# Kernel optimization log

Measured on AMD Instinct MI355X. Metric: run time of the kernel, lower is better.

## Reference

```python
import jax, jax.numpy as jnp
import numpy as np

D_MODEL = 1024  # scale uses sqrt(d_model), matching the source's sqrt(C)

def setup_inputs() -> dict:
    key = jax.random.key(0)
    kx, kq, kk, kv = jax.random.split(key, 4)
    B, T, C, H = 8, 2048, D_MODEL, 64
    s = 1.0 / np.sqrt(C)
    return {
        "x": jax.random.normal(kx, (B, T, C), dtype=jnp.float32),
        "Wq": jax.random.normal(kq, (C, H), dtype=jnp.float32) * s,
        "Wk": jax.random.normal(kk, (C, H), dtype=jnp.float32) * s,
        "Wv": jax.random.normal(kv, (C, H), dtype=jnp.float32) * s,
    }

def reference(x, Wq, Wk, Wv):
    B, T, C = x.shape
    q = jnp.einsum("btc,ch->bth", x, Wq)
    k = jnp.einsum("btc,ch->bth", x, Wk)
    v = jnp.einsum("btc,ch->bth", x, Wv)
    # scores scaled by 1/sqrt(C) (C = d_model), faithful to source
    wei = jnp.einsum("bth,bsh->bts", q, k) / jnp.sqrt(jnp.float32(C))
    causal = jnp.tril(jnp.ones((T, T), dtype=bool))  # [T, T]
    wei = jnp.where(causal, wei, -jnp.inf)
    wei = jax.nn.softmax(wei, axis=-1)
    out = jnp.einsum("bts,bsh->bth", wei, v)
    return out
```

## Files before the change

### kernel.cpp

```cpp
#include <hip/hip_runtime.h>

typedef unsigned short u16;
typedef __attribute__((ext_vector_type(4))) float f32x4;
typedef __attribute__((ext_vector_type(8))) short bf16x8;
typedef __attribute__((ext_vector_type(4))) u16 u16x4;

#define MFMA(a, b, c) __builtin_amdgcn_mfma_f32_16x16x32_bf16(a, b, c, 0, 0, 0)

__device__ __forceinline__ u16 f2bf(float f) {
    unsigned u = __float_as_uint(f);
    u += 0x7fffu + ((u >> 16) & 1u);
    return (u16)(u >> 16);
}

__device__ __forceinline__ void load_lds16(const void* g, void* l) {
    __builtin_amdgcn_global_load_lds((const __attribute__((address_space(1))) void*)g,
                                     (__attribute__((address_space(3))) void*)l,
                                     16, 0, 0);
}

__global__ void wt_pack(const float* __restrict__ Wq, const float* __restrict__ Wk,
                        const float* __restrict__ Wv, u16* __restrict__ Wtt) {
    const int k = blockIdx.x;
    const int n = threadIdx.x;
    const float* W = (n < 64) ? Wq : (n < 128 ? Wk : Wv);
    const float v = W[(size_t)k * 64 + (n & 63)];
    const int kt = k >> 6, ks = k & 63, c = ks >> 3, ci = ks & 7;
    Wtt[(size_t)kt * 12288 + n * 64 + (((c ^ (n & 7)) << 3) + ci)] = f2bf(v);
}

__global__ __launch_bounds__(256, 2) void qkv_gemm(const float* __restrict__ x,
                                                   const u16* __restrict__ Wtt,
                                                   u16* __restrict__ qo,
                                                   u16* __restrict__ ko,
                                                   u16* __restrict__ vT) {
    const int tid = threadIdx.x;
    const int lane = tid & 63, wave = tid >> 6;
    const int lr = lane & 15, lg = lane >> 4;
    const int m0 = blockIdx.x * 32;

    __shared__ __align__(16) float xs[2][32 * 64];
    __shared__ __align__(16) u16 ws[2][192 * 64];

    f32x4 acc[2][3];
#pragma unroll
    for (int m = 0; m < 2; ++m)
#pragma unroll
        for (int n = 0; n < 3; ++n) acc[m][n] = (f32x4){0.f, 0.f, 0.f, 0.f};

    const int srow = tid >> 4;
    const int schk = tid & 15;

    {
#pragma unroll
        for (int j = 0; j < 2; ++j) {
            const int rr = j * 16 + srow;
            const float* src = x + (size_t)(m0 + rr) * 1024 + ((schk ^ (rr & 7)) << 2);
            load_lds16(src, &xs[0][j * 1024 + wave * 256]);
        }
#pragma unroll
        for (int j = 0; j < 6; ++j) {
            const u16* src = Wtt + (size_t)j * 2048 + tid * 8;
            load_lds16(src, &ws[0][j * 2048 + wave * 512]);
        }
    }
    __syncthreads();

    for (int kt = 0; kt < 16; ++kt) {
        const int cur = kt & 1;
        if (kt < 15) {
            const int nxt = cur ^ 1;
#pragma unroll
            for (int j = 0; j < 2; ++j) {
                const int rr = j * 16 + srow;
                const float* src =
                    x + (size_t)(m0 + rr) * 1024 + (kt + 1) * 64 + ((schk ^ (rr & 7)) << 2);
                load_lds16(src, &xs[nxt][j * 1024 + wave * 256]);
            }
#pragma unroll
            for (int j = 0; j < 6; ++j) {
                const u16* src = Wtt + (size_t)(kt + 1) * 12288 + j * 2048 + tid * 8;
                load_lds16(src, &ws[nxt][j * 2048 + wave * 512]);
            }
        }
#pragma unroll
        for (int h = 0; h < 2; ++h) {
            bf16x8 a[2];
#pragma unroll
            for (int mm = 0; mm < 2; ++mm) {
                const int rr = mm * 16 + lr;
                const int c0 = h * 8 + lg * 2;
                f32x4 f0 = *(const f32x4*)&xs[cur][rr * 64 + ((c0 ^ (rr & 7)) << 2)];
                f32x4 f1 = *(const f32x4*)&xs[cur][rr * 64 + (((c0 + 1) ^ (rr & 7)) << 2)];
                bf16x8 t;
#pragma unroll
                for (int i = 0; i < 4; ++i) {
                    t[i] = (short)f2bf(f0[i]);
                    t[i + 4] = (short)f2bf(f1[i]);
                }
                a[mm] = t;
            }
#pragma unroll
            for (int nl = 0; nl < 3; ++nl) {
                const int row = (wave * 3 + nl) * 16 + lr;
                const int cb = h * 4 + lg;
                const bf16x8 b = *(const bf16x8*)&ws[cur][row * 64 + ((cb ^ (row & 7)) << 3)];
                acc[0][nl] = MFMA(a[0], b, acc[0][nl]);
                acc[1][nl] = MFMA(a[1], b, acc[1][nl]);
            }
        }
        __syncthreads();
    }

    const float SCQ = 0.0450842200277801f;
    const int bb = m0 >> 11;
    const int tb = m0 & 2047;
#pragma unroll
    for (int mm = 0; mm < 2; ++mm)
#pragma unroll
        for (int nl = 0; nl < 3; ++nl) {
            const int col = (wave * 3 + nl) * 16 + lr;
            const int rl = mm * 16 + lg * 4;
            if (col < 64) {
#pragma unroll
                for (int r = 0; r < 4; ++r)
                    qo[(size_t)(m0 + rl + r) * 64 + col] = f2bf(acc[mm][nl][r] * SCQ);
            } else if (col < 128) {
#pragma unroll
                for (int r = 0; r < 4; ++r)
                    ko[(size_t)(m0 + rl + r) * 64 + (col - 64)] = f2bf(acc[mm][nl][r]);
            } else {
                u16x4 pk;
#pragma unroll
                for (int r = 0; r < 4; ++r) pk[r] = f2bf(acc[mm][nl][r]);
                *(u16x4*)&vT[(size_t)(bb * 64 + (col - 128)) * 2048 + tb + rl] = pk;
            }
        }
}

#define PPITCH 72
__global__ __launch_bounds__(256, 2) void attn_part(const u16* __restrict__ q,
                                                    const u16* __restrict__ k,
                                                    const u16* __restrict__ vT,
                                                    float* __restrict__ Op,
                                                    float* __restrict__ Lp) {
    const int b = blockIdx.x & 7;
    int g = blockIdx.x >> 3;
    int qt = 31, rem = g;
    while (rem >= (qt >> 3) + 1) { rem -= (qt >> 3) + 1; --qt; }
    const int c0 = rem;
    const int q0 = qt * 64;
    const int kv_lo = c0 * 512;
    const int kv_hi = min(kv_lo + 512, q0 + 64);
    const int ntiles = (kv_hi - kv_lo) >> 6;
    const int slot = (b * 32 + qt) * 4 + c0;

    __shared__ __align__(16) u16 lK[2][64 * 64];
    __shared__ __align__(16) u16 lV[2][64 * 64];
    __shared__ __align__(16) u16 lP[4][16 * PPITCH];

    const int tid = threadIdx.x;
    const int wave = tid >> 6, lane = tid & 63;
    const int lr = lane & 15, lg = lane >> 4;

    const u16* qb = q + (size_t)b * 2048 * 64;
    const u16* kb = k + (size_t)b * 2048 * 64;
    const u16* vb = vT + (size_t)b * 64 * 2048;

    const int myrow = q0 + wave * 16 + lr;
    const bf16x8 qf0 = *(const bf16x8*)(qb + (size_t)myrow * 64 + lg * 8);
    const bf16x8 qf1 = *(const bf16x8*)(qb + (size_t)myrow * 64 + 32 + lg * 8);

    f32x4 oacc[4];
#pragma unroll
    for (int n = 0; n < 4; ++n) oacc[n] = (f32x4){0.f, 0.f, 0.f, 0.f};
    float rs = 0.f;

#define STAGE(bufi, kv0_)                                                             \
    {                                                                                 \
        _Pragma("unroll") for (int j = 0; j < 2; ++j) {                               \
            const int cid = j * 256 + wave * 64 + lane;                               \
            const int row = cid >> 3, cc = cid & 7;                                   \
            load_lds16(kb + (size_t)((kv0_) + row) * 64 + ((cc ^ (row & 7)) << 3),    \
                       &lK[bufi][(j * 256 + wave * 64) * 8]);                         \
            load_lds16(vb + (size_t)row * 2048 + (kv0_) + ((cc ^ (row & 7)) << 3),    \
                       &lV[bufi][(j * 256 + wave * 64) * 8]);                         \
        }                                                                             \
    }

    STAGE(0, kv_lo);
    __syncthreads();

    for (int it = 0; it < ntiles; ++it) {
        const int cur = it & 1;
        if (it + 1 < ntiles) STAGE(cur ^ 1, kv_lo + (it + 1) * 64);

        const int kv0 = kv_lo + it * 64;
        if (kv0 <= q0 + wave * 16 + 15) {
            f32x4 s[4];
#pragma unroll
            for (int n = 0; n < 4; ++n) {
                const int row = n * 16 + lr;
                const bf16x8 kf0 = *(const bf16x8*)&lK[cur][row * 64 + ((lg ^ (row & 7)) << 3)];
                const bf16x8 kf1 =
                    *(const bf16x8*)&lK[cur][row * 64 + (((4 + lg) ^ (row & 7)) << 3)];
                f32x4 a = (f32x4){0.f, 0.f, 0.f, 0.f};
                a = MFMA(kf0, qf0, a);
                a = MFMA(kf1, qf1, a);
                s[n] = a;
            }

            const bool msk = (kv0 + 63 > q0 + wave * 16);
#pragma unroll
            for (int n = 0; n < 4; ++n) {
                u16x4 pk;
#pragma unroll
                for (int r = 0; r < 4; ++r) {
                    const int kvi = kv0 + n * 16 + lg * 4 + r;
                    const float p = (!msk || kvi <= myrow) ? exp2f(s[n][r]) : 0.f;
                    rs += p;
                    pk[r] = f2bf(p);
                }
                *(u16x4*)&lP[wave][lr * PPITCH + n * 16 + lg * 4] = pk;
            }

#pragma unroll
            for (int kc = 0; kc < 2; ++kc) {
                const bf16x8 pf = *(const bf16x8*)&lP[wave][lr * PPITCH + kc * 32 + lg * 8];
#pragma unroll
                for (int n = 0; n < 4; ++n) {
                    const int row = n * 16 + lr;
                    const bf16x8 vf =
                        *(const bf16x8*)&lV[cur][row * 64 + (((kc * 4 + lg) ^ (row & 7)) << 3)];
                    oacc[n] = MFMA(pf, vf, oacc[n]);
                }
            }
        }
        __syncthreads();
    }

    rs += __shfl_xor(rs, 16);
    rs += __shfl_xor(rs, 32);
    if (lane < 16) Lp[slot * 64 + wave * 16 + lr] = rs;

    float* op = Op + (size_t)slot * 4096;
#pragma unroll
    for (int n = 0; n < 4; ++n)
#pragma unroll
        for (int r = 0; r < 4; ++r)
            op[(wave * 16 + lg * 4 + r) * 64 + n * 16 + lr] = oacc[n][r];
}

__global__ __launch_bounds__(256) void attn_combine(const float* __restrict__ Op,
                                                    const float* __restrict__ Lp,
                                                    float* __restrict__ out) {
    const int gid = blockIdx.x * 256 + threadIdx.x;
    const int col = gid & 63;
    const int row = gid >> 6;
    const int b = row >> 11, tt = row & 2047;
    const int qt = tt >> 6, i = tt & 63;
    const int nc = (qt >> 3) + 1;
    const size_t sbase = (size_t)(b * 32 + qt) * 4;

    float O = 0.f, L = 0.f;
    for (int c = 0; c < nc; ++c) {
        O += Op[(sbase + c) * 4096 + i * 64 + col];
        L += Lp[(sbase + c) * 64 + i];
    }
    out[(size_t)row * 64 + col] = O / L;
}

extern "C" void kernel_launch(void* const* d_in, const int* in_sizes, int n_in,
                              void* d_out, int out_size, void* d_ws, size_t ws_size,
                              hipStream_t stream) {
    const float* x = (const float*)d_in[0];
    const float* Wq = (const float*)d_in[1];
    const float* Wk = (const float*)d_in[2];
    const float* Wv = (const float*)d_in[3];
    float* out = (float*)d_out;

    char* ws = (char*)d_ws;
    u16* Wtt = (u16*)ws;
    u16* qb = (u16*)(ws + (512 << 10));
    u16* kb = (u16*)(ws + (512 << 10) + (2 << 20));
    u16* vT = (u16*)(ws + (512 << 10) + (4 << 20));
    float* Op = (float*)(ws + (8 << 20));
    float* Lp = (float*)(ws + (25 << 20));

    wt_pack<<<1024, 192, 0, stream>>>(Wq, Wk, Wv, Wtt);
    qkv_gemm<<<512, 256, 0, stream>>>(x, Wtt, qb, kb, vT);
    attn_part<<<640, 256, 0, stream>>>(qb, kb, vT, Op, Lp);
    attn_combine<<<4096, 256, 0, stream>>>(Op, Lp, out);
}
```

Baseline: 57.21 us.

## Enlarge GEMM and attention KV tiles and store partial outputs as bf16

The QKV GEMM now uses 512-thread blocks covering 64 rows, so each staged weight tile is shared by twice as many rows. The attention kernel stages 128 KV rows per iteration instead of 64, which halves the number of barriers and loop trips. Partial attention outputs are written as bf16 in a tiled layout, cutting the write and read traffic of the combine pass. The trade-offs are more LDS per block, which may lower occupancy, and some precision lost in the partial sums.

```diff
diff --git a/kernel.cpp b/kernel.cpp
--- a/kernel.cpp
+++ b/kernel.cpp
@@ -11,6 +11,10 @@
     unsigned u = __float_as_uint(f);
     u += 0x7fffu + ((u >> 16) & 1u);
     return (u16)(u >> 16);
+}
+__device__ __forceinline__ float bf2f(u16 h) {
+    unsigned u = ((unsigned)h) << 16;
+    return __uint_as_float(u);
 }
 
 __device__ __forceinline__ void load_lds16(const void* g, void* l) {
@@ -29,7 +33,7 @@
     Wtt[(size_t)kt * 12288 + n * 64 + (((c ^ (n & 7)) << 3) + ci)] = f2bf(v);
 }
 
-__global__ __launch_bounds__(256, 2) void qkv_gemm(const float* __restrict__ x,
+__global__ __launch_bounds__(512, 2) void qkv_gemm(const float* __restrict__ x,
                                                    const u16* __restrict__ Wtt,
                                                    u16* __restrict__ qo,
                                                    u16* __restrict__ ko,
@@ -37,9 +41,10 @@
     const int tid = threadIdx.x;
     const int lane = tid & 63, wave = tid >> 6;
     const int lr = lane & 15, lg = lane >> 4;
-    const int m0 = blockIdx.x * 32;
-
-    __shared__ __align__(16) float xs[2][32 * 64];
+    const int wr = wave >> 2, wc = wave & 3;
+    const int m0 = blockIdx.x * 64;
+
+    __shared__ __align__(16) float xs[2][64 * 64];
     __shared__ __align__(16) u16 ws[2][192 * 64];
 
     f32x4 acc[2][3];
@@ -48,47 +53,34 @@
 #pragma unroll
         for (int n = 0; n < 3; ++n) acc[m][n] = (f32x4){0.f, 0.f, 0.f, 0.f};
 
-    const int srow = tid >> 4;
-    const int schk = tid & 15;
-
-    {
-#pragma unroll
-        for (int j = 0; j < 2; ++j) {
-            const int rr = j * 16 + srow;
-            const float* src = x + (size_t)(m0 + rr) * 1024 + ((schk ^ (rr & 7)) << 2);
-            load_lds16(src, &xs[0][j * 1024 + wave * 256]);
-        }
-#pragma unroll
-        for (int j = 0; j < 6; ++j) {
-            const u16* src = Wtt + (size_t)j * 2048 + tid * 8;
-            load_lds16(src, &ws[0][j * 2048 + wave * 512]);
-        }
-    }
+#define QSTAGE(bufi, kt_)                                                              \
+    {                                                                                  \
+        _Pragma("unroll") for (int j = 0; j < 2; ++j) {                                \
+            const int cid = j * 512 + tid;                                             \
+            const int row = cid >> 4, cc = cid & 15;                                   \
+            load_lds16(x + (size_t)(m0 + row) * 1024 + (kt_)*64 +                      \
+                           ((cc ^ (row & 7)) << 2),                                    \
+                       &xs[bufi][(j * 512 + wave * 64) * 4]);                          \
+        }                                                                              \
+        _Pragma("unroll") for (int j = 0; j < 3; ++j) {                                \
+            const int cid = j * 512 + tid;                                             \
+            load_lds16(Wtt + (size_t)(kt_)*12288 + cid * 8,                            \
+                       &ws[bufi][(j * 512 + wave * 64) * 8]);                          \
+        }                                                                              \
+    }
+
+    QSTAGE(0, 0);
     __syncthreads();
 
     for (int kt = 0; kt < 16; ++kt) {
         const int cur = kt & 1;
-        if (kt < 15) {
-            const int nxt = cur ^ 1;
-#pragma unroll
-            for (int j = 0; j < 2; ++j) {
-                const int rr = j * 16 + srow;
-                const float* src =
-                    x + (size_t)(m0 + rr) * 1024 + (kt + 1) * 64 + ((schk ^ (rr & 7)) << 2);
-                load_lds16(src, &xs[nxt][j * 1024 + wave * 256]);
-            }
-#pragma unroll
-            for (int j = 0; j < 6; ++j) {
-                const u16* src = Wtt + (size_t)(kt + 1) * 12288 + j * 2048 + tid * 8;
-                load_lds16(src, &ws[nxt][j * 2048 + wave * 512]);
-            }
-        }
+        if (kt < 15) QSTAGE(cur ^ 1, kt + 1);
 #pragma unroll
         for (int h = 0; h < 2; ++h) {
             bf16x8 a[2];
 #pragma unroll
             for (int mm = 0; mm < 2; ++mm) {
-                const int rr = mm * 16 + lr;
+                const int rr = wr * 32 + mm * 16 + lr;
                 const int c0 = h * 8 + lg * 2;
                 f32x4 f0 = *(const f32x4*)&xs[cur][rr * 64 + ((c0 ^ (rr & 7)) << 2)];
                 f32x4 f1 = *(const f32x4*)&xs[cur][rr * 64 + (((c0 + 1) ^ (rr & 7)) << 2)];
@@ -102,7 +94,7 @@
             }
 #pragma unroll
             for (int nl = 0; nl < 3; ++nl) {
-                const int row = (wave * 3 + nl) * 16 + lr;
+                const int row = wc * 48 + nl * 16 + lr;
                 const int cb = h * 4 + lg;
                 const bf16x8 b = *(const bf16x8*)&ws[cur][row * 64 + ((cb ^ (row & 7)) << 3)];
                 acc[0][nl] = MFMA(a[0], b, acc[0][nl]);
@@ -119,8 +111,8 @@
     for (int mm = 0; mm < 2; ++mm)
 #pragma unroll
         for (int nl = 0; nl < 3; ++nl) {
-            const int col = (wave * 3 + nl) * 16 + lr;
-            const int rl = mm * 16 + lg * 4;
+            const int col = wc * 48 + nl * 16 + lr;
+            const int rl = wr * 32 + mm * 16 + lg * 4;
             if (col < 64) {
 #pragma unroll
                 for (int r = 0; r < 4; ++r)
@@ -142,7 +134,7 @@
 __global__ __launch_bounds__(256, 2) void attn_part(const u16* __restrict__ q,
                                                     const u16* __restrict__ k,
                                                     const u16* __restrict__ vT,
-                                                    float* __restrict__ Op,
+                                                    u16* __restrict__ Opb,
                                                     float* __restrict__ Lp) {
     const int b = blockIdx.x & 7;
     int g = blockIdx.x >> 3;
@@ -152,11 +144,11 @@
     const int q0 = qt * 64;
     const int kv_lo = c0 * 512;
     const int kv_hi = min(kv_lo + 512, q0 + 64);
-    const int ntiles = (kv_hi - kv_lo) >> 6;
+    const int niter = (kv_hi - kv_lo + 127) >> 7;
     const int slot = (b * 32 + qt) * 4 + c0;
 
-    __shared__ __align__(16) u16 lK[2][64 * 64];
-    __shared__ __align__(16) u16 lV[2][64 * 64];
+    __shared__ __align__(16) u16 lK[2][128 * 64];
+    __shared__ __align__(16) u16 lV[2][64 * 128];
     __shared__ __align__(16) u16 lP[4][16 * PPITCH];
 
     const int tid = threadIdx.x;
@@ -176,63 +168,71 @@
     for (int n = 0; n < 4; ++n) oacc[n] = (f32x4){0.f, 0.f, 0.f, 0.f};
     float rs = 0.f;
 
-#define STAGE(bufi, kv0_)                                                             \
-    {                                                                                 \
-        _Pragma("unroll") for (int j = 0; j < 2; ++j) {                               \
-            const int cid = j * 256 + wave * 64 + lane;                               \
-            const int row = cid >> 3, cc = cid & 7;                                   \
-            load_lds16(kb + (size_t)((kv0_) + row) * 64 + ((cc ^ (row & 7)) << 3),    \
-                       &lK[bufi][(j * 256 + wave * 64) * 8]);                         \
-            load_lds16(vb + (size_t)row * 2048 + (kv0_) + ((cc ^ (row & 7)) << 3),    \
-                       &lV[bufi][(j * 256 + wave * 64) * 8]);                         \
-        }                                                                             \
-    }
-
-    STAGE(0, kv_lo);
+#define ASTAGE(bufi, kv0_)                                                             \
+    {                                                                                  \
+        _Pragma("unroll") for (int j = 0; j < 4; ++j) {                                \
+            const int cid = j * 256 + tid;                                             \
+            const int krow = cid >> 3, kcc = cid & 7;                                  \
+            load_lds16(kb + (size_t)((kv0_) + krow) * 64 + ((kcc ^ (krow & 7)) << 3),  \
+                       &lK[bufi][(j * 256 + wave * 64) * 8]);                          \
+            const int vrow = cid >> 4, vcc = cid & 15;                                 \
+            const int vsw = (vcc & 8) | ((vcc & 7) ^ (vrow & 7));                      \
+            load_lds16(vb + (size_t)vrow * 2048 + (kv0_) + (vsw << 3),                 \
+                       &lV[bufi][(j * 256 + wave * 64) * 8]);                          \
+        }                                                                              \
+    }
+
+    ASTAGE(0, kv_lo);
     __syncthreads();
 
-    for (int it = 0; it < ntiles; ++it) {
+    for (int it = 0; it < niter; ++it) {
         const int cur = it & 1;
-        if (it + 1 < ntiles) STAGE(cur ^ 1, kv_lo + (it + 1) * 64);
-
-        const int kv0 = kv_lo + it * 64;
-        if (kv0 <= q0 + wave * 16 + 15) {
-            f32x4 s[4];
-#pragma unroll
-            for (int n = 0; n < 4; ++n) {
-                const int row = n * 16 + lr;
-                const bf16x8 kf0 = *(const bf16x8*)&lK[cur][row * 64 + ((lg ^ (row & 7)) << 3)];
-                const bf16x8 kf1 =
-                    *(const bf16x8*)&lK[cur][row * 64 + (((4 + lg) ^ (row & 7)) << 3)];
-                f32x4 a = (f32x4){0.f, 0.f, 0.f, 0.f};
-                a = MFMA(kf0, qf0, a);
-                a = MFMA(kf1, qf1, a);
-                s[n] = a;
-            }
-
-            const bool msk = (kv0 + 63 > q0 + wave * 16);
-#pragma unroll
-            for (int n = 0; n < 4; ++n) {
-                u16x4 pk;
-#pragma unroll
-                for (int r = 0; r < 4; ++r) {
-                    const int kvi = kv0 + n * 16 + lg * 4 + r;
-                    const float p = (!msk || kvi <= myrow) ? exp2f(s[n][r]) : 0.f;
-                    rs += p;
-                    pk[r] = f2bf(p);
-                }
-                *(u16x4*)&lP[wave][lr * PPITCH + n * 16 + lg * 4] = pk;
-            }
-
-#pragma unroll
-            for (int kc = 0; kc < 2; ++kc) {
-                const bf16x8 pf = *(const bf16x8*)&lP[wave][lr * PPITCH + kc * 32 + lg * 8];
+        if (it + 1 < niter) ASTAGE(cur ^ 1, kv_lo + (it + 1) * 128);
+
+#pragma unroll
+        for (int hh = 0; hh < 2; ++hh) {
+            const int kv0 = kv_lo + it * 128 + hh * 64;
+            if (kv0 < kv_hi && kv0 <= q0 + wave * 16 + 15) {
+                f32x4 s[4];
 #pragma unroll
                 for (int n = 0; n < 4; ++n) {
-                    const int row = n * 16 + lr;
-                    const bf16x8 vf =
-                        *(const bf16x8*)&lV[cur][row * 64 + (((kc * 4 + lg) ^ (row & 7)) << 3)];
-                    oacc[n] = MFMA(pf, vf, oacc[n]);
+                    const int row = hh * 64 + n * 16 + lr;
+                    const bf16x8 kf0 =
+                        *(const bf16x8*)&lK[cur][row * 64 + ((lg ^ (row & 7)) << 3)];
+                    const bf16x8 kf1 =
+                        *(const bf16x8*)&lK[cur][row * 64 + (((4 + lg) ^ (row & 7)) << 3)];
+                    f32x4 a = (f32x4){0.f, 0.f, 0.f, 0.f};
+                    a = MFMA(kf0, qf0, a);
+                    a = MFMA(kf1, qf1, a);
+                    s[n] = a;
+                }
+
+                const bool msk = (kv0 + 63 > q0 + wave * 16);
+#pragma unroll
+                for (int n = 0; n < 4; ++n) {
+                    u16x4 pk;
+#pragma unroll
+                    for (int r = 0; r < 4; ++r) {
+                        const int kvi = kv0 + n * 16 + lg * 4 + r;
+                        const float p = (!msk || kvi <= myrow) ? exp2f(s[n][r]) : 0.f;
+                        rs += p;
+                        pk[r] = f2bf(p);
+                    }
+                    *(u16x4*)&lP[wave][lr * PPITCH + n * 16 + lg * 4] = pk;
+                }
+
+#pragma unroll
+                for (int kc = 0; kc < 2; ++kc) {
+                    const bf16x8 pf =
+                        *(const bf16x8*)&lP[wave][lr * PPITCH + kc * 32 + lg * 8];
+#pragma unroll
+                    for (int n = 0; n < 4; ++n) {
+                        const int row = n * 16 + lr;
+                        const int c = hh * 8 + kc * 4 + lg;
+                        const int csw = (c & 8) | ((c & 7) ^ (row & 7));
+                        const bf16x8 vf = *(const bf16x8*)&lV[cur][row * 128 + (csw << 3)];
+                        oacc[n] = MFMA(pf, vf, oacc[n]);
+                    }
                 }
             }
         }
@@ -243,15 +243,15 @@
     rs += __shfl_xor(rs, 32);
     if (lane < 16) Lp[slot * 64 + wave * 16 + lr] = rs;
 
-    float* op = Op + (size_t)slot * 4096;
+    u16* op = Opb + (size_t)slot * 4096 + wave * 1024;
 #pragma unroll
     for (int n = 0; n < 4; ++n)
 #pragma unroll
         for (int r = 0; r < 4; ++r)
-            op[(wave * 16 + lg * 4 + r) * 64 + n * 16 + lr] = oacc[n][r];
-}
-
-__global__ __launch_bounds__(256) void attn_combine(const float* __restrict__ Op,
+            op[n * 256 + (lg * 4 + r) * 16 + lr] = f2bf(oacc[n][r]);
+}
+
+__global__ __launch_bounds__(256) void attn_combine(const u16* __restrict__ Opb,
                                                     const float* __restrict__ Lp,
                                                     float* __restrict__ out) {
     const int gid = blockIdx.x * 256 + threadIdx.x;
@@ -261,10 +261,11 @@
     const int qt = tt >> 6, i = tt & 63;
     const int nc = (qt >> 3) + 1;
     const size_t sbase = (size_t)(b * 32 + qt) * 4;
+    const int sub = (i >> 4) * 1024 + (col >> 4) * 256 + (i & 15) * 16 + (col & 15);
 
     float O = 0.f, L = 0.f;
     for (int c = 0; c < nc; ++c) {
-        O += Op[(sbase + c) * 4096 + i * 64 + col];
+        O += bf2f(Opb[(sbase + c) * 4096 + sub]);
         L += Lp[(sbase + c) * 64 + i];
     }
     out[(size_t)row * 64 + col] = O / L;
@@ -284,11 +285,11 @@
     u16* qb = (u16*)(ws + (512 << 10));
     u16* kb = (u16*)(ws + (512 << 10) + (2 << 20));
     u16* vT = (u16*)(ws + (512 << 10) + (4 << 20));
-    float* Op = (float*)(ws + (8 << 20));
-    float* Lp = (float*)(ws + (25 << 20));
+    u16* Opb = (u16*)(ws + (8 << 20));
+    float* Lp = (float*)(ws + (20 << 20));
 
     wt_pack<<<1024, 192, 0, stream>>>(Wq, Wk, Wv, Wtt);
-    qkv_gemm<<<512, 256, 0, stream>>>(x, Wtt, qb, kb, vT);
-    attn_part<<<640, 256, 0, stream>>>(qb, kb, vT, Op, Lp);
-    attn_combine<<<4096, 256, 0, stream>>>(Op, Lp, out);
-}
+    qkv_gemm<<<256, 512, 0, stream>>>(x, Wtt, qb, kb, vT);
+    attn_part<<<640, 256, 0, stream>>>(qb, kb, vT, Opb, Lp);
+    attn_combine<<<4096, 256, 0, stream>>>(Opb, Lp, out);
+}
```

Result: slower. 60.61 us (+5.9%).

## Triple-buffer K/V staging with vmcnt waits and store bf16 partial outputs

Applied to the files above, without the earlier changes.

The attention kernel moves from double to triple-buffered K/V tiles in LDS. It issues the prefetch two tiles ahead and uses explicit vmcnt waits plus raw barriers, replacing a full __syncthreads per tile, to overlap loads with MFMA work. Partial output accumulators are now written as bf16 in a wave-blocked layout, which the combine kernel reads with matching indexing. This halves partial-result traffic at the cost of bf16 rounding of unnormalized partial sums. LDS use per block also grows.

```diff
diff --git a/kernel.cpp b/kernel.cpp
--- a/kernel.cpp
+++ b/kernel.cpp
@@ -11,6 +11,10 @@
     unsigned u = __float_as_uint(f);
     u += 0x7fffu + ((u >> 16) & 1u);
     return (u16)(u >> 16);
+}
+__device__ __forceinline__ float bf2f(u16 h) {
+    unsigned u = ((unsigned)h) << 16;
+    return __uint_as_float(u);
 }
 
 __device__ __forceinline__ void load_lds16(const void* g, void* l) {
@@ -142,7 +146,7 @@
 __global__ __launch_bounds__(256, 2) void attn_part(const u16* __restrict__ q,
                                                     const u16* __restrict__ k,
                                                     const u16* __restrict__ vT,
-                                                    float* __restrict__ Op,
+                                                    u16* __restrict__ Opb,
                                                     float* __restrict__ Lp) {
     const int b = blockIdx.x & 7;
     int g = blockIdx.x >> 3;
@@ -152,11 +156,11 @@
     const int q0 = qt * 64;
     const int kv_lo = c0 * 512;
     const int kv_hi = min(kv_lo + 512, q0 + 64);
-    const int ntiles = (kv_hi - kv_lo) >> 6;
+    const int niter = (kv_hi - kv_lo) >> 6;
     const int slot = (b * 32 + qt) * 4 + c0;
 
-    __shared__ __align__(16) u16 lK[2][64 * 64];
-    __shared__ __align__(16) u16 lV[2][64 * 64];
+    __shared__ __align__(16) u16 lK[3][64 * 64];
+    __shared__ __align__(16) u16 lV[3][64 * 64];
     __shared__ __align__(16) u16 lP[4][16 * PPITCH];
 
     const int tid = threadIdx.x;
@@ -176,26 +180,32 @@
     for (int n = 0; n < 4; ++n) oacc[n] = (f32x4){0.f, 0.f, 0.f, 0.f};
     float rs = 0.f;
 
-#define STAGE(bufi, kv0_)                                                             \
-    {                                                                                 \
-        _Pragma("unroll") for (int j = 0; j < 2; ++j) {                               \
-            const int cid = j * 256 + wave * 64 + lane;                               \
-            const int row = cid >> 3, cc = cid & 7;                                   \
-            load_lds16(kb + (size_t)((kv0_) + row) * 64 + ((cc ^ (row & 7)) << 3),    \
-                       &lK[bufi][(j * 256 + wave * 64) * 8]);                         \
-            load_lds16(vb + (size_t)row * 2048 + (kv0_) + ((cc ^ (row & 7)) << 3),    \
-                       &lV[bufi][(j * 256 + wave * 64) * 8]);                         \
-        }                                                                             \
-    }
-
-    STAGE(0, kv_lo);
-    __syncthreads();
-
-    for (int it = 0; it < ntiles; ++it) {
-        const int cur = it & 1;
-        if (it + 1 < ntiles) STAGE(cur ^ 1, kv_lo + (it + 1) * 64);
-
+#define ASTAGE(bufi, kv0_)                                                             \
+    {                                                                                  \
+        _Pragma("unroll") for (int j = 0; j < 2; ++j) {                                \
+            const int cid = j * 256 + wave * 64 + lane;                                \
+            const int row = cid >> 3, cc = cid & 7;                                    \
+            load_lds16(kb + (size_t)((kv0_) + row) * 64 + ((cc ^ (row & 7)) << 3),     \
+                       &lK[bufi][(j * 256 + wave * 64) * 8]);                          \
+            load_lds16(vb + (size_t)row * 2048 + (kv0_) + ((cc ^ (row & 7)) << 3),     \
+                       &lV[bufi][(j * 256 + wave * 64) * 8]);                          \
+        }                                                                              \
+    }
+
+    ASTAGE(0, kv_lo);
+    if (niter > 1) {
+        ASTAGE(1, kv_lo + 64);
+        asm volatile("s_waitcnt vmcnt(4)" ::: "memory");
+    } else {
+        asm volatile("s_waitcnt vmcnt(0)" ::: "memory");
+    }
+    __builtin_amdgcn_s_barrier();
+    __builtin_amdgcn_sched_barrier(0);
+
+    for (int it = 0; it < niter; ++it) {
+        const int cur = it % 3;
         const int kv0 = kv_lo + it * 64;
+
         if (kv0 <= q0 + wave * 16 + 15) {
             f32x4 s[4];
 #pragma unroll
@@ -236,22 +246,33 @@
                 }
             }
         }
-        __syncthreads();
+
+        if (it + 2 < niter) ASTAGE((it + 2) % 3, kv_lo + (it + 2) * 64);
+
+        if (it + 1 < niter) {
+            if (it + 2 < niter) {
+                asm volatile("s_waitcnt vmcnt(4)" ::: "memory");
+            } else {
+                asm volatile("s_waitcnt vmcnt(0)" ::: "memory");
+            }
+            __builtin_amdgcn_s_barrier();
+            __builtin_amdgcn_sched_barrier(0);
+        }
     }
 
     rs += __shfl_xor(rs, 16);
     rs += __shfl_xor(rs, 32);
     if (lane < 16) Lp[slot * 64 + wave * 16 + lr] = rs;
 
-    float* op = Op + (size_t)slot * 4096;
+    u16* op = Opb + (size_t)slot * 4096 + wave * 1024;
 #pragma unroll
     for (int n = 0; n < 4; ++n)
 #pragma unroll
         for (int r = 0; r < 4; ++r)
-            op[(wave * 16 + lg * 4 + r) * 64 + n * 16 + lr] = oacc[n][r];
-}
-
-__global__ __launch_bounds__(256) void attn_combine(const float* __restrict__ Op,
+            op[n * 256 + (lg * 4 + r) * 16 + lr] = f2bf(oacc[n][r]);
+}
+
+__global__ __launch_bounds__(256) void attn_combine(const u16* __restrict__ Opb,
                                                     const float* __restrict__ Lp,
                                                     float* __restrict__ out) {
     const int gid = blockIdx.x * 256 + threadIdx.x;
@@ -261,10 +282,11 @@
     const int qt = tt >> 6, i = tt & 63;
     const int nc = (qt >> 3) + 1;
     const size_t sbase = (size_t)(b * 32 + qt) * 4;
+    const int sub = (i >> 4) * 1024 + (col >> 4) * 256 + (i & 15) * 16 + (col & 15);
 
     float O = 0.f, L = 0.f;
     for (int c = 0; c < nc; ++c) {
-        O += Op[(sbase + c) * 4096 + i * 64 + col];
+        O += bf2f(Opb[(sbase + c) * 4096 + sub]);
         L += Lp[(sbase + c) * 64 + i];
     }
     out[(size_t)row * 64 + col] = O / L;
@@ -284,11 +306,11 @@
     u16* qb = (u16*)(ws + (512 << 10));
     u16* kb = (u16*)(ws + (512 << 10) + (2 << 20));
     u16* vT = (u16*)(ws + (512 << 10) + (4 << 20));
-    float* Op = (float*)(ws + (8 << 20));
-    float* Lp = (float*)(ws + (25 << 20));
+    u16* Opb = (u16*)(ws + (8 << 20));
+    float* Lp = (float*)(ws + (20 << 20));
 
     wt_pack<<<1024, 192, 0, stream>>>(Wq, Wk, Wv, Wtt);
     qkv_gemm<<<512, 256, 0, stream>>>(x, Wtt, qb, kb, vT);
-    attn_part<<<640, 256, 0, stream>>>(qb, kb, vT, Op, Lp);
-    attn_combine<<<4096, 256, 0, stream>>>(Op, Lp, out);
-}
+    attn_part<<<640, 256, 0, stream>>>(qb, kb, vT, Opb, Lp);
+    attn_combine<<<4096, 256, 0, stream>>>(Opb, Lp, out);
+}
```

Result: slower. 60.94 us (+6.5%).
